# Kernel optimization log

Measured on AMD Instinct MI355X. Metric: run time of the kernel, lower is better.

## Reference

```python
import jax, jax.numpy as jnp
import numpy as np

Q_HEADS = 16
KV_HEADS = 4
ROPE_THETA = 10000.0


def _rope(x, seq_len):
    # x: [B, S, H, D]; pairs are consecutive along D (view_as_complex semantics)
    D = x.shape[-1]
    inv_freq = 1.0 / (ROPE_THETA ** (jnp.arange(0, D, 2, dtype=jnp.float32) / D))
    freqs = jnp.arange(seq_len, dtype=jnp.float32)[:, None] * inv_freq  # [S, D/2]
    cos = jnp.cos(freqs)[None, :, None, :]
    sin = jnp.sin(freqs)[None, :, None, :]
    xr = x.reshape(x.shape[:-1] + (D // 2, 2))
    x0, x1 = xr[..., 0], xr[..., 1]
    out = jnp.stack([x0 * cos - x1 * sin, x0 * sin + x1 * cos], axis=-1)
    return out.reshape(x.shape)


def setup_inputs() -> dict:
    key = jax.random.key(0)
    ks = jax.random.split(key, 6)
    B, S, E = 1, 2048, 2048
    KV_DIM = KV_HEADS * (E // Q_HEADS)  # 512
    scale = 0.02
    return {
        "x": jax.random.normal(ks[0], (B, S, E), dtype=jnp.float32),
        "Wq": jax.random.normal(ks[1], (E, E), dtype=jnp.float32) * scale,
        "Wk": jax.random.normal(ks[2], (KV_DIM, E), dtype=jnp.float32) * scale,
        "Wv": jax.random.normal(ks[3], (KV_DIM, E), dtype=jnp.float32) * scale,
        "Wo": jax.random.normal(ks[4], (E, E), dtype=jnp.float32) * scale,
        "bo": jax.random.normal(ks[5], (E,), dtype=jnp.float32) * scale,
        "cache_keys": jnp.zeros((B, S, KV_HEADS, E // Q_HEADS), dtype=jnp.float32),
        "cache_value": jnp.zeros((B, S, KV_HEADS, E // Q_HEADS), dtype=jnp.float32),
        "start_pos": 0,
    }


def reference(x, Wq, Wk, Wv, Wo, bo, cache_keys, cache_value, start_pos):
    B, S, E = x.shape
    hd = E // Q_HEADS
    G = Q_HEADS // KV_HEADS  # queries per kv head

    xq = (x @ Wq.T).reshape(B, S, Q_HEADS, hd)
    xk = (x @ Wk.T).reshape(B, S, KV_HEADS, hd)
    xv = (x @ Wv.T).reshape(B, S, KV_HEADS, hd)

    # Original applies RoPE with positions 0..seq_len-1 for both q and k
    # (freq tensor is sliced [:seq_len] inside apply_rotry_position_embedding).
    xq = _rope(xq, S)
    xk = _rope(xk, S)

    # cache write at start_pos (static python int)
    cache_keys = jax.lax.dynamic_update_slice(cache_keys, xk, (0, start_pos, 0, 0))
    cache_value = jax.lax.dynamic_update_slice(cache_value, xv, (0, start_pos, 0, 0))
    total = start_pos + S
    k_full = cache_keys[:, :total]   # [B, T, KVH, hd]
    v_full = cache_value[:, :total]

    # repeat_interleave over the head axis == GQA expansion
    k = jnp.repeat(k_full, G, axis=2)  # [B, T, QH, hd]
    v = jnp.repeat(v_full, G, axis=2)

    scores = jnp.einsum("bshd,bthd->bhst", xq, k) / jnp.sqrt(jnp.float32(hd))
    causal = jnp.triu(jnp.ones((S, total), dtype=bool), k=1)  # [S, T]
    scores = jnp.where(causal[None, None, :, :], -jnp.inf, scores)
    weights = jax.nn.softmax(scores, axis=-1)
    out = jnp.einsum("bhst,bthd->bshd", weights, v).reshape(B, S, E)
    # dropout p=0.0 / eval mode -> identity
    return out @ Wo.T + bo
```

## Files before the change

kernel.cpp:

```cpp
#include <hip/hip_runtime.h>
#include <stdint.h>

typedef unsigned short u16;
typedef float  f32x4  __attribute__((ext_vector_type(4)));
typedef __bf16 bf16x8 __attribute__((ext_vector_type(8)));
typedef __bf16 bf16x4 __attribute__((ext_vector_type(4)));
typedef unsigned short u16x8 __attribute__((ext_vector_type(8)));
typedef unsigned short u16x4v __attribute__((ext_vector_type(4)));

#define S_LEN 2048
#define E_DIM 2048
#define HD    128
#define QH    16
#define KVH   4
#define KVD   512
#define NQKV  3072
#define QK_SCALE 0.08838834764831845f

#define AS1 __attribute__((address_space(1)))
#define AS3 __attribute__((address_space(3)))

__device__ __forceinline__ u16 f2bf(float f) {
  union { float f; uint32_t u; } v; v.f = f;
  return (u16)((v.u + 0x7FFFu + ((v.u >> 16) & 1u)) >> 16);
}
__device__ __forceinline__ float bf2f(u16 b) {
  union { uint32_t u; float f; } v; v.u = ((uint32_t)b) << 16;
  return v.f;
}

__global__ void cast_all_kernel(const float* __restrict__ x, const float* __restrict__ Wq,
                                const float* __restrict__ Wk, const float* __restrict__ Wv,
                                const float* __restrict__ Wo,
                                u16* __restrict__ xb, u16* __restrict__ Wcat,
                                u16* __restrict__ Wob) {
  int i = blockIdx.x * blockDim.x + threadIdx.x;
  const float* src; u16* dst;
  if (i < (1 << 20))                       { src = x  + (size_t)i * 4;  dst = xb + (size_t)i * 4; }
  else if (i < (2 << 20))                  { size_t j = i - (1 << 20);  src = Wq + j * 4; dst = Wcat + j * 4; }
  else if (i < (2 << 20) + (1 << 18))      { size_t j = i - (2 << 20);  src = Wk + j * 4; dst = Wcat + (size_t)E_DIM * E_DIM + j * 4; }
  else if (i < (2 << 20) + (2 << 18))      { size_t j = i - (2 << 20) - (1 << 18); src = Wv + j * 4; dst = Wcat + (size_t)(E_DIM + KVD) * E_DIM + j * 4; }
  else                                     { size_t j = i - (2 << 20) - (2 << 18); src = Wo + j * 4; dst = Wob + j * 4; }
  float4 f = *reinterpret_cast<const float4*>(src);
  u16x4v o;
  o[0] = f2bf(f.x); o[1] = f2bf(f.y); o[2] = f2bf(f.z); o[3] = f2bf(f.w);
  *reinterpret_cast<u16x4v*>(dst) = o;
}

template<bool BIAS, bool OBF16>
__global__ __launch_bounds__(256) void gemm_bt_kernel(
    const u16* __restrict__ A, const u16* __restrict__ B,
    void* __restrict__ Cv, const float* __restrict__ bias,
    int M, int N, int K)
{
  __shared__ u16 As[2][128 * 64];
  __shared__ u16 Bs[2][128 * 64];

  const int tid  = threadIdx.x;
  const int lane = tid & 63;
  const int wid  = tid >> 6;
  const int wr   = (wid >> 1) * 64;
  const int wc   = (wid & 1) * 64;
  const int lr   = lane & 15;
  const int kg   = lane >> 4;

  const int bm = blockIdx.y * 128;
  const int bn = blockIdx.x * 128;

  f32x4 acc[4][4];
  #pragma unroll
  for (int r = 0; r < 4; ++r)
    #pragma unroll
    for (int c = 0; c < 4; ++c) acc[r][c] = (f32x4){0.f, 0.f, 0.f, 0.f};

  const int l8 = lane & 7;
  const int l3 = lane >> 3;
  const int schunk = l8 ^ l3;

  const u16* gA = A + (size_t)(bm + wid*32 + l3) * K + schunk * 8;
  const u16* gB = B + (size_t)(bn + wid*32 + l3) * K + schunk * 8;

  const int sw = lr & 7;

  auto stage = [&](int buf, int kt) {
    #pragma unroll
    for (int i = 0; i < 4; ++i) {
      __builtin_amdgcn_global_load_lds(
          (const AS1 void*)(gA + (size_t)i * 8 * K + kt),
          (AS3 void*)(&As[buf][wid*32*64 + i*8*64]), 16, 0, 0);
      __builtin_amdgcn_global_load_lds(
          (const AS1 void*)(gB + (size_t)i * 8 * K + kt),
          (AS3 void*)(&Bs[buf][wid*32*64 + i*8*64]), 16, 0, 0);
    }
  };

  stage(0, 0);
  __syncthreads();

  int cur = 0;
  for (int kt = 0; kt < K; kt += 64) {
    if (kt + 64 < K) stage(cur ^ 1, kt + 64);
    #pragma unroll
    for (int kk = 0; kk < 2; ++kk) {
      bf16x8 af[4], bfr[4];
      #pragma unroll
      for (int r = 0; r < 4; ++r)
        af[r] = *reinterpret_cast<const bf16x8*>(
            &As[cur][(wr + r*16 + lr)*64 + ((kk*4 + kg) ^ sw)*8]);
      #pragma unroll
      for (int c = 0; c < 4; ++c)
        bfr[c] = *reinterpret_cast<const bf16x8*>(
            &Bs[cur][(wc + c*16 + lr)*64 + ((kk*4 + kg) ^ sw)*8]);
      #pragma unroll
      for (int r = 0; r < 4; ++r)
        #pragma unroll
        for (int c = 0; c < 4; ++c)
          acc[r][c] = __builtin_amdgcn_mfma_f32_16x16x32_bf16(af[r], bfr[c], acc[r][c], 0, 0, 0);
    }
    __syncthreads();
    cur ^= 1;
  }

  const int crow = kg * 4;
  #pragma unroll
  for (int r = 0; r < 4; ++r) {
    #pragma unroll
    for (int c = 0; c < 4; ++c) {
      int gr = bm + wr + r*16 + crow;
      int gc = bn + wc + c*16 + lr;
      float badd = BIAS ? bias[gc] : 0.0f;
      #pragma unroll
      for (int reg = 0; reg < 4; ++reg) {
        float v = acc[r][c][reg] + badd;
        if constexpr (OBF16)
          ((u16*)Cv)[(size_t)(gr + reg)*N + gc] = f2bf(v);
        else
          ((float*)Cv)[(size_t)(gr + reg)*N + gc] = v;
      }
    }
  }
}

__global__ void rope_split_kernel(const u16* __restrict__ qkv,
                                  u16* __restrict__ qb, u16* __restrict__ kb) {
  int idx = blockIdx.x * blockDim.x + threadIdx.x;
  int s  = idx / 1280;
  int cp = idx - s * 1280;
  int col = cp * 2;
  const u16* src = qkv + (size_t)s * NQKV + col;
  float x0 = bf2f(src[0]), x1 = bf2f(src[1]);
  int p = (col & 127) >> 1;
  float inv = exp2f((float)p * (-13.287712379549449f / 64.0f));
  float ang = (float)s * inv;
  float sn, cs;
  sincosf(ang, &sn, &cs);
  float o0 = x0 * cs - x1 * sn;
  float o1 = x0 * sn + x1 * cs;
  if (col < E_DIM) {
    o0 *= QK_SCALE; o1 *= QK_SCALE;
    qb[(size_t)s * E_DIM + col]     = f2bf(o0);
    qb[(size_t)s * E_DIM + col + 1] = f2bf(o1);
  } else {
    kb[(size_t)s * KVD + (col - E_DIM)]     = f2bf(o0);
    kb[(size_t)s * KVD + (col - E_DIM) + 1] = f2bf(o1);
  }
}

__global__ void transpose_v_kernel(const u16* __restrict__ qkv, u16* __restrict__ vT) {
  __shared__ u16 tile[32][33];
  const int sbase = blockIdx.x * 32;
  const int cbase = blockIdx.y * 32;
  const int tx = threadIdx.x;
  const int ty = threadIdx.y;
  #pragma unroll
  for (int i = 0; i < 32; i += 8)
    tile[ty + i][tx] = qkv[(size_t)(sbase + ty + i) * NQKV + (E_DIM + KVD) + cbase + tx];
  __syncthreads();
  #pragma unroll
  for (int i = 0; i < 32; i += 8)
    vT[(size_t)(cbase + ty + i) * S_LEN + sbase + tx] = tile[tx][ty + i];
}

__global__ __launch_bounds__(256, 2) void attn_kernel(
    const u16* __restrict__ Q, const u16* __restrict__ Kc,
    const u16* __restrict__ VT, u16* __restrict__ Out)
{
  __shared__ u16 Ks[2][64 * 128];
  __shared__ u16 VTs[128 * 64];
  __shared__ u16 Ps[4][16 * 72];

  const int x    = blockIdx.x;
  const int pp   = x >> 1;
  const int base = pp & 15;
  const int h    = (pp >> 4) & 15;
  const int flip = (x ^ (x >> 8)) & 1;
  const int qt   = flip ? 31 - base : base;
  const int kvh  = h >> 2;

  const int tid  = threadIdx.x;
  const int lane = tid & 63;
  const int wid  = tid >> 6;
  const int lr   = lane & 15;
  const int kg   = lane >> 4;
  const int sw   = lr & 7;

  const int NT = qt + 1;

  bf16x8 qf[4];
  {
    const u16* qa = Q + (size_t)(qt*64 + wid*16 + lr) * E_DIM + h * HD + kg * 8;
    #pragma unroll
    for (int kk = 0; kk < 4; ++kk)
      qf[kk] = *reinterpret_cast<const bf16x8*>(qa + kk * 32);
  }

  f32x4 o[8];
  #pragma unroll
  for (int d = 0; d < 8; ++d) o[d] = (f32x4){0.f,0.f,0.f,0.f};
  float mr = -1e30f, ls = 0.f;

  const u16* kbase = Kc + kvh * HD;
  const u16* vbase = VT + (size_t)(kvh * HD) * S_LEN;
  u16* ps = Ps[wid];

  const int kr_off = lane >> 4;
  const int kchunk = lane & 15;
  auto k_dma = [&](int buf, int t) {
    #pragma unroll
    for (int j = 0; j < 4; ++j) {
      int r0 = j*16 + wid*4;
      int r  = r0 + kr_off;
      const u16* src = kbase + (size_t)(t*64 + r) * KVD + ((kchunk ^ (r & 7)) * 8);
      __builtin_amdgcn_global_load_lds((const AS1 void*)src,
          (AS3 void*)(&Ks[buf][r0 * 128]), 16, 0, 0);
    }
  };

  u16x8 vreg[4];
  auto v_load = [&](int t) {
    #pragma unroll
    for (int i = 0; i < 4; ++i) {
      int c = i * 256 + tid;
      vreg[i] = *reinterpret_cast<const u16x8*>(
          vbase + (size_t)(c >> 3) * S_LEN + t*64 + (c & 7) * 8);
    }
  };
  auto v_write = [&]() {
    #pragma unroll
    for (int i = 0; i < 4; ++i) {
      int c = i * 256 + tid;
      int d = c >> 3;
      *reinterpret_cast<u16x8*>(&VTs[d*64 + ((c & 7) ^ (d & 7)) * 8]) = vreg[i];
    }
  };

  k_dma(0, 0);
  v_load(0);
  v_write();
  __syncthreads();

  int p = 0;
  for (int t = 0; t < NT; ++t) {
    const bool lastt = (t + 1 == NT);
    if (!lastt) { k_dma(p ^ 1, t + 1); v_load(t + 1); }

    f32x4 st[4];
    #pragma unroll
    for (int c = 0; c < 4; ++c) st[c] = (f32x4){0.f, 0.f, 0.f, 0.f};
    __builtin_amdgcn_s_setprio(1);
    #pragma unroll
    for (int kk = 0; kk < 4; ++kk) {
      #pragma unroll
      for (int c = 0; c < 4; ++c) {
        bf16x8 kfr = *reinterpret_cast<const bf16x8*>(
            &Ks[p][(c*16 + lr)*128 + ((kk*4 + kg) ^ sw)*8]);
        st[c] = __builtin_amdgcn_mfma_f32_16x16x32_bf16(kfr, qf[kk], st[c], 0, 0, 0);
      }
    }
    __builtin_amdgcn_s_setprio(0);

    if (t == qt) {
      #pragma unroll
      for (int c = 0; c < 4; ++c)
        #pragma unroll
        for (int reg = 0; reg < 4; ++reg)
          if (c*16 + kg*4 + reg > wid*16 + lr) st[c][reg] = -1e30f;
    }

    float cm[4];
    #pragma unroll
    for (int c = 0; c < 4; ++c)
      cm[c] = fmaxf(fmaxf(st[c][0], st[c][1]), fmaxf(st[c][2], st[c][3]));
    float pm = fmaxf(fmaxf(cm[0], cm[1]), fmaxf(cm[2], cm[3]));
    pm = fmaxf(pm, __shfl_xor(pm, 16));
    pm = fmaxf(pm, __shfl_xor(pm, 32));

    if (!__all(pm - mr <= 8.0f)) {
      float nm = fmaxf(mr, pm);
      float alpha = __expf(mr - nm);
      ls *= alpha;
      mr = nm;
      float ar[4];
      #pragma unroll
      for (int reg = 0; reg < 4; ++reg)
        ar[reg] = __shfl(alpha, kg*4 + reg);
      #pragma unroll
      for (int d = 0; d < 8; ++d)
        #pragma unroll
        for (int reg = 0; reg < 4; ++reg)
          o[d][reg] *= ar[reg];
    }

    float sum = 0.f;
    #pragma unroll
    for (int c = 0; c < 4; ++c) {
      float pr[4];
      #pragma unroll
      for (int reg = 0; reg < 4; ++reg)
        pr[reg] = __expf(st[c][reg] - mr);
      sum += (pr[0] + pr[1]) + (pr[2] + pr[3]);
      bf16x4 pk;
      #pragma unroll
      for (int reg = 0; reg < 4; ++reg) pk[reg] = (__bf16)pr[reg];
      *reinterpret_cast<bf16x4*>(&ps[lr*72 + c*16 + kg*4]) = pk;
    }
    sum += __shfl_xor(sum, 16);
    sum += __shfl_xor(sum, 32);
    ls += sum;

    bf16x8 pa[2];
    #pragma unroll
    for (int kk = 0; kk < 2; ++kk)
      pa[kk] = *reinterpret_cast<const bf16x8*>(&ps[lr*72 + kk*32 + kg*8]);
    __builtin_amdgcn_s_setprio(1);
    #pragma unroll
    for (int d0 = 0; d0 < 8; ++d0) {
      #pragma unroll
      for (int kk = 0; kk < 2; ++kk) {
        bf16x8 vb = *reinterpret_cast<const bf16x8*>(
            &VTs[(d0*16 + lr)*64 + ((kk*4 + kg) ^ sw)*8]);
        o[d0] = __builtin_amdgcn_mfma_f32_16x16x32_bf16(pa[kk], vb, o[d0], 0, 0, 0);
      }
    }
    __builtin_amdgcn_s_setprio(0);

    if (!lastt) {
      __syncthreads();
      v_write();
      __syncthreads();
      p ^= 1;
    }
  }

  {
    float inv = 1.0f / ls;
    float ivq[4];
    #pragma unroll
    for (int reg = 0; reg < 4; ++reg)
      ivq[reg] = __shfl(inv, kg*4 + reg);
    #pragma unroll
    for (int reg = 0; reg < 4; ++reg) {
      int grow = qt*64 + wid*16 + kg*4 + reg;
      #pragma unroll
      for (int d = 0; d < 8; ++d)
        Out[(size_t)grow * E_DIM + h * HD + d*16 + lr] =
            __builtin_bit_cast(u16, (__bf16)(o[d][reg] * ivq[reg]));
    }
  }
}

extern "C" void kernel_launch(void* const* d_in, const int* in_sizes, int n_in,
                              void* d_out, int out_size, void* d_ws, size_t ws_size,
                              hipStream_t stream)
{
  const float* x  = (const float*)d_in[0];
  const float* Wq = (const float*)d_in[1];
  const float* Wk = (const float*)d_in[2];
  const float* Wv = (const float*)d_in[3];
  const float* Wo = (const float*)d_in[4];
  const float* bo = (const float*)d_in[5];
  float* out = (float*)d_out;

  char* w = (char*)d_ws;
  u16*   xb   = (u16*)(w);
  u16*   Wcat = (u16*)(w + (8u  << 20));
  u16*   Wob  = (u16*)(w + (20u << 20));
  u16*   qkv  = (u16*)(w + (28u << 20));
  u16*   qb   = (u16*)(w + (52u << 20));
  u16*   kb   = (u16*)(w + (60u << 20));
  u16*   vT   = (u16*)(w + (62u << 20));
  u16*   attn = (u16*)(w + (64u << 20));
  (void)ws_size; (void)in_sizes; (void)n_in; (void)out_size;

  cast_all_kernel<<<14336, 256, 0, stream>>>(x, Wq, Wk, Wv, Wo, xb, Wcat, Wob);

  gemm_bt_kernel<false, true><<<dim3(NQKV/128, S_LEN/128), 256, 0, stream>>>(
      xb, Wcat, qkv, nullptr, S_LEN, NQKV, E_DIM);

  rope_split_kernel<<<(S_LEN * 1280) / 256, 256, 0, stream>>>(qkv, qb, kb);
  transpose_v_kernel<<<dim3(S_LEN/32, KVD/32), dim3(32, 8), 0, stream>>>(qkv, vT);

  attn_kernel<<<512, 256, 0, stream>>>(qb, kb, vT, attn);

  gemm_bt_kernel<true, false><<<dim3(E_DIM/128, S_LEN/128), 256, 0, stream>>>(
      attn, Wob, out, bo, S_LEN, E_DIM, E_DIM);
}
```

Baseline: 151.5 us.

## Split KV tiles across two wave groups per attention block and merge

```diff
diff --git a/kernel.cpp b/kernel.cpp
--- a/kernel.cpp
+++ b/kernel.cpp
@@ -181,34 +181,37 @@
     vT[(size_t)(cbase + ty + i) * S_LEN + sbase + tx] = tile[tx][ty + i];
 }
 
-__global__ __launch_bounds__(256, 2) void attn_kernel(
+__global__ __launch_bounds__(512, 1) void attn_kernel(
     const u16* __restrict__ Q, const u16* __restrict__ Kc,
     const u16* __restrict__ VT, u16* __restrict__ Out)
 {
-  __shared__ u16 Ks[2][64 * 128];
-  __shared__ u16 VTs[128 * 64];
-  __shared__ u16 Ps[4][16 * 72];
-
-  const int x    = blockIdx.x;
-  const int pp   = x >> 1;
-  const int base = pp & 15;
-  const int h    = (pp >> 4) & 15;
-  const int flip = (x ^ (x >> 8)) & 1;
-  const int qt   = flip ? 31 - base : base;
-  const int kvh  = h >> 2;
+  __shared__ u16 Ks[2][2][64 * 128];
+  __shared__ u16 VTs[2][128 * 64];
+  __shared__ u16 Ps[8][16 * 72];
+  __shared__ float Lm[4][16], Ll[4][16];
+
+  const int x = blockIdx.x;
+  int qt, h;
+  if (x < 256) { qt = 31 - (x & 15); h = x >> 4; }
+  else         { int y = x - 256; qt = 15 - (y & 15); h = y >> 4; }
+  const int kvh = h >> 2;
 
   const int tid  = threadIdx.x;
   const int lane = tid & 63;
   const int wid  = tid >> 6;
+  const int grp  = wid >> 2;
+  const int wl   = wid & 3;
+  const int ltid = tid & 255;
   const int lr   = lane & 15;
   const int kg   = lane >> 4;
   const int sw   = lr & 7;
 
   const int NT = qt + 1;
+  const int NI = (NT + 1) >> 1;
 
   bf16x8 qf[4];
   {
-    const u16* qa = Q + (size_t)(qt*64 + wid*16 + lr) * E_DIM + h * HD + kg * 8;
+    const u16* qa = Q + (size_t)(qt*64 + wl*16 + lr) * E_DIM + h * HD + kg * 8;
     #pragma unroll
     for (int kk = 0; kk < 4; ++kk)
       qf[kk] = *reinterpret_cast<const bf16x8*>(qa + kk * 32);
@@ -228,11 +231,11 @@
   auto k_dma = [&](int buf, int t) {
     #pragma unroll
     for (int j = 0; j < 4; ++j) {
-      int r0 = j*16 + wid*4;
+      int r0 = j*16 + wl*4;
       int r  = r0 + kr_off;
       const u16* src = kbase + (size_t)(t*64 + r) * KVD + ((kchunk ^ (r & 7)) * 8);
       __builtin_amdgcn_global_load_lds((const AS1 void*)src,
-          (AS3 void*)(&Ks[buf][r0 * 128]), 16, 0, 0);
+          (AS3 void*)(&Ks[grp][buf][r0 * 128]), 16, 0, 0);
     }
   };
 
@@ -240,7 +243,7 @@
   auto v_load = [&](int t) {
     #pragma unroll
     for (int i = 0; i < 4; ++i) {
-      int c = i * 256 + tid;
+      int c = i * 256 + ltid;
       vreg[i] = *reinterpret_cast<const u16x8*>(
           vbase + (size_t)(c >> 3) * S_LEN + t*64 + (c & 7) * 8);
     }
@@ -248,123 +251,151 @@
   auto v_write = [&]() {
     #pragma unroll
     for (int i = 0; i < 4; ++i) {
-      int c = i * 256 + tid;
+      int c = i * 256 + ltid;
       int d = c >> 3;
-      *reinterpret_cast<u16x8*>(&VTs[d*64 + ((c & 7) ^ (d & 7)) * 8]) = vreg[i];
+      *reinterpret_cast<u16x8*>(&VTs[grp][d*64 + ((c & 7) ^ (d & 7)) * 8]) = vreg[i];
     }
   };
 
-  k_dma(0, 0);
-  v_load(0);
-  v_write();
+  if (grp < NT) {
+    k_dma(0, grp);
+    v_load(grp);
+    v_write();
+  }
   __syncthreads();
 
   int p = 0;
-  for (int t = 0; t < NT; ++t) {
-    const bool lastt = (t + 1 == NT);
-    if (!lastt) { k_dma(p ^ 1, t + 1); v_load(t + 1); }
-
-    f32x4 st[4];
-    #pragma unroll
-    for (int c = 0; c < 4; ++c) st[c] = (f32x4){0.f, 0.f, 0.f, 0.f};
-    __builtin_amdgcn_s_setprio(1);
-    #pragma unroll
-    for (int kk = 0; kk < 4; ++kk) {
+  for (int i = 0; i < NI; ++i) {
+    const int t = 2*i + grp;
+    const bool valid = t < NT;
+    const bool hn = t + 2 < NT;
+    if (valid && hn) { k_dma(p ^ 1, t + 2); v_load(t + 2); }
+
+    if (valid) {
+      f32x4 st[4];
+      #pragma unroll
+      for (int c = 0; c < 4; ++c) st[c] = (f32x4){0.f, 0.f, 0.f, 0.f};
+      __builtin_amdgcn_s_setprio(1);
+      #pragma unroll
+      for (int kk = 0; kk < 4; ++kk) {
+        #pragma unroll
+        for (int c = 0; c < 4; ++c) {
+          bf16x8 kfr = *reinterpret_cast<const bf16x8*>(
+              &Ks[grp][p][(c*16 + lr)*128 + ((kk*4 + kg) ^ sw)*8]);
+          st[c] = __builtin_amdgcn_mfma_f32_16x16x32_bf16(kfr, qf[kk], st[c], 0, 0, 0);
+        }
+      }
+      __builtin_amdgcn_s_setprio(0);
+
+      if (t == qt) {
+        #pragma unroll
+        for (int c = 0; c < 4; ++c)
+          #pragma unroll
+          for (int reg = 0; reg < 4; ++reg)
+            if (c*16 + kg*4 + reg > wl*16 + lr) st[c][reg] = -1e30f;
+      }
+
+      float cm[4];
+      #pragma unroll
+      for (int c = 0; c < 4; ++c)
+        cm[c] = fmaxf(fmaxf(st[c][0], st[c][1]), fmaxf(st[c][2], st[c][3]));
+      float pm = fmaxf(fmaxf(cm[0], cm[1]), fmaxf(cm[2], cm[3]));
+      pm = fmaxf(pm, __shfl_xor(pm, 16));
+      pm = fmaxf(pm, __shfl_xor(pm, 32));
+
+      if (!__all(pm - mr <= 8.0f)) {
+        float nm = fmaxf(mr, pm);
+        float alpha = __expf(mr - nm);
+        ls *= alpha;
+        mr = nm;
+        float ar[4];
+        #pragma unroll
+        for (int reg = 0; reg < 4; ++reg)
+          ar[reg] = __shfl(alpha, kg*4 + reg);
+        #pragma unroll
+        for (int d = 0; d < 8; ++d)
+          #pragma unroll
+          for (int reg = 0; reg < 4; ++reg)
+            o[d][reg] *= ar[reg];
+      }
+
+      float sum = 0.f;
       #pragma unroll
       for (int c = 0; c < 4; ++c) {
-        bf16x8 kfr = *reinterpret_cast<const bf16x8*>(
-            &Ks[p][(c*16 + lr)*128 + ((kk*4 + kg) ^ sw)*8]);
-        st[c] = __builtin_amdgcn_mfma_f32_16x16x32_bf16(kfr, qf[kk], st[c], 0, 0, 0);
-      }
-    }
-    __builtin_amdgcn_s_setprio(0);
-
-    if (t == qt) {
-      #pragma unroll
-      for (int c = 0; c < 4; ++c)
+        float pr[4];
         #pragma unroll
         for (int reg = 0; reg < 4; ++reg)
-          if (c*16 + kg*4 + reg > wid*16 + lr) st[c][reg] = -1e30f;
-    }
-
-    float cm[4];
-    #pragma unroll
-    for (int c = 0; c < 4; ++c)
-      cm[c] = fmaxf(fmaxf(st[c][0], st[c][1]), fmaxf(st[c][2], st[c][3]));
-    float pm = fmaxf(fmaxf(cm[0], cm[1]), fmaxf(cm[2], cm[3]));
-    pm = fmaxf(pm, __shfl_xor(pm, 16));
-    pm = fmaxf(pm, __shfl_xor(pm, 32));
-
-    if (!__all(pm - mr <= 8.0f)) {
-      float nm = fmaxf(mr, pm);
-      float alpha = __expf(mr - nm);
-      ls *= alpha;
-      mr = nm;
-      float ar[4];
-      #pragma unroll
-      for (int reg = 0; reg < 4; ++reg)
-        ar[reg] = __shfl(alpha, kg*4 + reg);
-      #pragma unroll
-      for (int d = 0; d < 8; ++d)
-        #pragma unroll
-        for (int reg = 0; reg < 4; ++reg)
-          o[d][reg] *= ar[reg];
-    }
-
-    float sum = 0.f;
-    #pragma unroll
-    for (int c = 0; c < 4; ++c) {
-      float pr[4];
-      #pragma unroll
-      for (int reg = 0; reg < 4; ++reg)
-        pr[reg] = __expf(st[c][reg] - mr);
-      sum += (pr[0] + pr[1]) + (pr[2] + pr[3]);
-      bf16x4 pk;
-      #pragma unroll
-      for (int reg = 0; reg < 4; ++reg) pk[reg] = (__bf16)pr[reg];
-      *reinterpret_cast<bf16x4*>(&ps[lr*72 + c*16 + kg*4]) = pk;
-    }
-    sum += __shfl_xor(sum, 16);
-    sum += __shfl_xor(sum, 32);
-    ls += sum;
-
-    bf16x8 pa[2];
-    #pragma unroll
-    for (int kk = 0; kk < 2; ++kk)
-      pa[kk] = *reinterpret_cast<const bf16x8*>(&ps[lr*72 + kk*32 + kg*8]);
-    __builtin_amdgcn_s_setprio(1);
-    #pragma unroll
-    for (int d0 = 0; d0 < 8; ++d0) {
-      #pragma unroll
-      for (int kk = 0; kk < 2; ++kk) {
-        bf16x8 vb = *reinterpret_cast<const bf16x8*>(
-            &VTs[(d0*16 + lr)*64 + ((kk*4 + kg) ^ sw)*8]);
-        o[d0] = __builtin_amdgcn_mfma_f32_16x16x32_bf16(pa[kk], vb, o[d0], 0, 0, 0);
-      }
-    }
-    __builtin_amdgcn_s_setprio(0);
-
-    if (!lastt) {
+          pr[reg] = __expf(st[c][reg] - mr);
+        sum += (pr[0] + pr[1]) + (pr[2] + pr[3]);
+        bf16x4 pk;
+        #pragma unroll
+        for (int reg = 0; reg < 4; ++reg) pk[reg] = (__bf16)pr[reg];
+        *reinterpret_cast<bf16x4*>(&ps[lr*72 + c*16 + kg*4]) = pk;
+      }
+      sum += __shfl_xor(sum, 16);
+      sum += __shfl_xor(sum, 32);
+      ls += sum;
+
+      bf16x8 pa[2];
+      #pragma unroll
+      for (int kk = 0; kk < 2; ++kk)
+        pa[kk] = *reinterpret_cast<const bf16x8*>(&ps[lr*72 + kk*32 + kg*8]);
+      __builtin_amdgcn_s_setprio(1);
+      #pragma unroll
+      for (int d0 = 0; d0 < 8; ++d0) {
+        #pragma unroll
+        for (int kk = 0; kk < 2; ++kk) {
+          bf16x8 vb = *reinterpret_cast<const bf16x8*>(
+              &VTs[grp][(d0*16 + lr)*64 + ((kk*4 + kg) ^ sw)*8]);
+          o[d0] = __builtin_amdgcn_mfma_f32_16x16x32_bf16(pa[kk], vb, o[d0], 0, 0, 0);
+        }
+      }
+      __builtin_amdgcn_s_setprio(0);
+    }
+
+    if (i + 1 < NI) {
       __syncthreads();
-      v_write();
+      if (hn) v_write();
       __syncthreads();
       p ^= 1;
     }
   }
 
-  {
-    float inv = 1.0f / ls;
-    float ivq[4];
-    #pragma unroll
-    for (int reg = 0; reg < 4; ++reg)
-      ivq[reg] = __shfl(inv, kg*4 + reg);
+  __syncthreads();
+  float* Obuf = (float*)&Ks[0][0][0];
+  if (grp == 1) {
+    if (kg == 0) { Lm[wl][lr] = mr; Ll[wl][lr] = ls; }
     #pragma unroll
     for (int reg = 0; reg < 4; ++reg) {
-      int grow = qt*64 + wid*16 + kg*4 + reg;
+      int rrow = wl*16 + kg*4 + reg;
       #pragma unroll
       for (int d = 0; d < 8; ++d)
+        Obuf[rrow*128 + d*16 + lr] = o[d][reg];
+    }
+  }
+  __syncthreads();
+  if (grp == 0) {
+    float m0r[4], l0r[4];
+    #pragma unroll
+    for (int reg = 0; reg < 4; ++reg) {
+      m0r[reg] = __shfl(mr, kg*4 + reg);
+      l0r[reg] = __shfl(ls, kg*4 + reg);
+    }
+    #pragma unroll
+    for (int reg = 0; reg < 4; ++reg) {
+      int rloc = kg*4 + reg;
+      float m1 = Lm[wl][rloc], l1 = Ll[wl][rloc];
+      float m  = fmaxf(m0r[reg], m1);
+      float a0 = __expf(m0r[reg] - m);
+      float a1 = __expf(m1 - m);
+      float inv = 1.0f / (l0r[reg]*a0 + l1*a1);
+      int grow = qt*64 + wl*16 + rloc;
+      #pragma unroll
+      for (int d = 0; d < 8; ++d) {
+        float v = (o[d][reg]*a0 + Obuf[(wl*16 + rloc)*128 + d*16 + lr]*a1) * inv;
         Out[(size_t)grow * E_DIM + h * HD + d*16 + lr] =
-            __builtin_bit_cast(u16, (__bf16)(o[d][reg] * ivq[reg]));
+            __builtin_bit_cast(u16, (__bf16)v);
+      }
     }
   }
 }
@@ -400,7 +431,7 @@
   rope_split_kernel<<<(S_LEN * 1280) / 256, 256, 0, stream>>>(qkv, qb, kb);
   transpose_v_kernel<<<dim3(S_LEN/32, KVD/32), dim3(32, 8), 0, stream>>>(qkv, vT);
 
-  attn_kernel<<<512, 256, 0, stream>>>(qb, kb, vT, attn);
+  attn_kernel<<<512, 512, 0, stream>>>(qb, kb, vT, attn);
 
   gemm_bt_kernel<true, false><<<dim3(E_DIM/128, S_LEN/128), 256, 0, stream>>>(
       attn, Wob, out, bo, S_LEN, E_DIM, E_DIM);
```

After: 161.5 us. +6.6%, slower.

## Switch attention to 32x32x16 MFMA with two waves per block

Applied to the files above, without the earlier changes.

```diff
diff --git a/kernel.cpp b/kernel.cpp
--- a/kernel.cpp
+++ b/kernel.cpp
@@ -3,6 +3,7 @@
 
 typedef unsigned short u16;
 typedef float  f32x4  __attribute__((ext_vector_type(4)));
+typedef float  f32x16 __attribute__((ext_vector_type(16)));
 typedef __bf16 bf16x8 __attribute__((ext_vector_type(8)));
 typedef __bf16 bf16x4 __attribute__((ext_vector_type(4)));
 typedef unsigned short u16x8 __attribute__((ext_vector_type(8)));
@@ -181,13 +182,13 @@
     vT[(size_t)(cbase + ty + i) * S_LEN + sbase + tx] = tile[tx][ty + i];
 }
 
-__global__ __launch_bounds__(256, 2) void attn_kernel(
+__global__ __launch_bounds__(128) void attn_kernel(
     const u16* __restrict__ Q, const u16* __restrict__ Kc,
     const u16* __restrict__ VT, u16* __restrict__ Out)
 {
   __shared__ u16 Ks[2][64 * 128];
   __shared__ u16 VTs[128 * 64];
-  __shared__ u16 Ps[4][16 * 72];
+  __shared__ u16 Ps[2][32 * 72];
 
   const int x    = blockIdx.x;
   const int pp   = x >> 1;
@@ -200,23 +201,24 @@
   const int tid  = threadIdx.x;
   const int lane = tid & 63;
   const int wid  = tid >> 6;
-  const int lr   = lane & 15;
-  const int kg   = lane >> 4;
-  const int sw   = lr & 7;
+  const int ln   = lane & 31;
+  const int hi   = lane >> 5;
 
   const int NT = qt + 1;
 
-  bf16x8 qf[4];
+  bf16x8 qf[8];
   {
-    const u16* qa = Q + (size_t)(qt*64 + wid*16 + lr) * E_DIM + h * HD + kg * 8;
-    #pragma unroll
-    for (int kk = 0; kk < 4; ++kk)
-      qf[kk] = *reinterpret_cast<const bf16x8*>(qa + kk * 32);
-  }
-
-  f32x4 o[8];
+    const u16* qa = Q + (size_t)(qt*64 + wid*32 + ln) * E_DIM + h * HD + hi * 8;
+    #pragma unroll
+    for (int ks = 0; ks < 8; ++ks)
+      qf[ks] = *reinterpret_cast<const bf16x8*>(qa + ks * 16);
+  }
+
+  f32x16 o4[4];
   #pragma unroll
-  for (int d = 0; d < 8; ++d) o[d] = (f32x4){0.f,0.f,0.f,0.f};
+  for (int d = 0; d < 4; ++d)
+    #pragma unroll
+    for (int r = 0; r < 16; ++r) o4[d][r] = 0.f;
   float mr = -1e30f, ls = 0.f;
 
   const u16* kbase = Kc + kvh * HD;
@@ -227,8 +229,8 @@
   const int kchunk = lane & 15;
   auto k_dma = [&](int buf, int t) {
     #pragma unroll
-    for (int j = 0; j < 4; ++j) {
-      int r0 = j*16 + wid*4;
+    for (int j = 0; j < 8; ++j) {
+      int r0 = j*8 + wid*4;
       int r  = r0 + kr_off;
       const u16* src = kbase + (size_t)(t*64 + r) * KVD + ((kchunk ^ (r & 7)) * 8);
       __builtin_amdgcn_global_load_lds((const AS1 void*)src,
@@ -236,19 +238,19 @@
     }
   };
 
-  u16x8 vreg[4];
+  u16x8 vreg[8];
   auto v_load = [&](int t) {
     #pragma unroll
-    for (int i = 0; i < 4; ++i) {
-      int c = i * 256 + tid;
+    for (int i = 0; i < 8; ++i) {
+      int c = i * 128 + tid;
       vreg[i] = *reinterpret_cast<const u16x8*>(
           vbase + (size_t)(c >> 3) * S_LEN + t*64 + (c & 7) * 8);
     }
   };
   auto v_write = [&]() {
     #pragma unroll
-    for (int i = 0; i < 4; ++i) {
-      int c = i * 256 + tid;
+    for (int i = 0; i < 8; ++i) {
+      int c = i * 128 + tid;
       int d = c >> 3;
       *reinterpret_cast<u16x8*>(&VTs[d*64 + ((c & 7) ^ (d & 7)) * 8]) = vreg[i];
     }
@@ -264,35 +266,39 @@
     const bool lastt = (t + 1 == NT);
     if (!lastt) { k_dma(p ^ 1, t + 1); v_load(t + 1); }
 
-    f32x4 st[4];
-    #pragma unroll
-    for (int c = 0; c < 4; ++c) st[c] = (f32x4){0.f, 0.f, 0.f, 0.f};
+    f32x16 st[2];
+    #pragma unroll
+    for (int c = 0; c < 2; ++c)
+      #pragma unroll
+      for (int r = 0; r < 16; ++r) st[c][r] = 0.f;
     __builtin_amdgcn_s_setprio(1);
     #pragma unroll
-    for (int kk = 0; kk < 4; ++kk) {
-      #pragma unroll
-      for (int c = 0; c < 4; ++c) {
+    for (int ks = 0; ks < 8; ++ks) {
+      #pragma unroll
+      for (int c = 0; c < 2; ++c) {
+        int row = c*32 + ln;
         bf16x8 kfr = *reinterpret_cast<const bf16x8*>(
-            &Ks[p][(c*16 + lr)*128 + ((kk*4 + kg) ^ sw)*8]);
-        st[c] = __builtin_amdgcn_mfma_f32_16x16x32_bf16(kfr, qf[kk], st[c], 0, 0, 0);
+            &Ks[p][row*128 + ((ks*2 + hi) ^ (row & 7))*8]);
+        st[c] = __builtin_amdgcn_mfma_f32_32x32x16_bf16(kfr, qf[ks], st[c], 0, 0, 0);
       }
     }
     __builtin_amdgcn_s_setprio(0);
 
     if (t == qt) {
       #pragma unroll
-      for (int c = 0; c < 4; ++c)
+      for (int c = 0; c < 2; ++c)
         #pragma unroll
-        for (int reg = 0; reg < 4; ++reg)
-          if (c*16 + kg*4 + reg > wid*16 + lr) st[c][reg] = -1e30f;
-    }
-
-    float cm[4];
-    #pragma unroll
-    for (int c = 0; c < 4; ++c)
-      cm[c] = fmaxf(fmaxf(st[c][0], st[c][1]), fmaxf(st[c][2], st[c][3]));
-    float pm = fmaxf(fmaxf(cm[0], cm[1]), fmaxf(cm[2], cm[3]));
-    pm = fmaxf(pm, __shfl_xor(pm, 16));
+        for (int reg = 0; reg < 16; ++reg) {
+          int kvl = c*32 + (reg & 3) + 8*(reg >> 2) + 4*hi;
+          if (kvl > wid*32 + ln) st[c][reg] = -1e30f;
+        }
+    }
+
+    float pm = -1e30f;
+    #pragma unroll
+    for (int c = 0; c < 2; ++c)
+      #pragma unroll
+      for (int reg = 0; reg < 16; ++reg) pm = fmaxf(pm, st[c][reg]);
     pm = fmaxf(pm, __shfl_xor(pm, 32));
 
     if (!__all(pm - mr <= 8.0f)) {
@@ -300,46 +306,47 @@
       float alpha = __expf(mr - nm);
       ls *= alpha;
       mr = nm;
-      float ar[4];
-      #pragma unroll
-      for (int reg = 0; reg < 4; ++reg)
-        ar[reg] = __shfl(alpha, kg*4 + reg);
-      #pragma unroll
-      for (int d = 0; d < 8; ++d)
+      #pragma unroll
+      for (int reg = 0; reg < 16; ++reg) {
+        int crow = (reg & 3) + 8*(reg >> 2) + 4*hi;
+        float ar = __shfl(alpha, crow);
         #pragma unroll
-        for (int reg = 0; reg < 4; ++reg)
-          o[d][reg] *= ar[reg];
+        for (int d = 0; d < 4; ++d) o4[d][reg] *= ar;
+      }
     }
 
     float sum = 0.f;
     #pragma unroll
-    for (int c = 0; c < 4; ++c) {
-      float pr[4];
-      #pragma unroll
-      for (int reg = 0; reg < 4; ++reg)
-        pr[reg] = __expf(st[c][reg] - mr);
-      sum += (pr[0] + pr[1]) + (pr[2] + pr[3]);
-      bf16x4 pk;
-      #pragma unroll
-      for (int reg = 0; reg < 4; ++reg) pk[reg] = (__bf16)pr[reg];
-      *reinterpret_cast<bf16x4*>(&ps[lr*72 + c*16 + kg*4]) = pk;
-    }
-    sum += __shfl_xor(sum, 16);
+    for (int c = 0; c < 2; ++c) {
+      #pragma unroll
+      for (int rg = 0; rg < 4; ++rg) {
+        float pr[4];
+        #pragma unroll
+        for (int j = 0; j < 4; ++j)
+          pr[j] = __expf(st[c][rg*4 + j] - mr);
+        sum += (pr[0] + pr[1]) + (pr[2] + pr[3]);
+        bf16x4 pk;
+        #pragma unroll
+        for (int j = 0; j < 4; ++j) pk[j] = (__bf16)pr[j];
+        *reinterpret_cast<bf16x4*>(&ps[ln*72 + c*32 + rg*8 + hi*4]) = pk;
+      }
+    }
     sum += __shfl_xor(sum, 32);
     ls += sum;
 
-    bf16x8 pa[2];
-    #pragma unroll
-    for (int kk = 0; kk < 2; ++kk)
-      pa[kk] = *reinterpret_cast<const bf16x8*>(&ps[lr*72 + kk*32 + kg*8]);
+    bf16x8 pa[4];
+    #pragma unroll
+    for (int ks = 0; ks < 4; ++ks)
+      pa[ks] = *reinterpret_cast<const bf16x8*>(&ps[ln*72 + ks*16 + hi*8]);
     __builtin_amdgcn_s_setprio(1);
     #pragma unroll
-    for (int d0 = 0; d0 < 8; ++d0) {
-      #pragma unroll
-      for (int kk = 0; kk < 2; ++kk) {
+    for (int d = 0; d < 4; ++d) {
+      #pragma unroll
+      for (int ks = 0; ks < 4; ++ks) {
+        int row = d*32 + ln;
         bf16x8 vb = *reinterpret_cast<const bf16x8*>(
-            &VTs[(d0*16 + lr)*64 + ((kk*4 + kg) ^ sw)*8]);
-        o[d0] = __builtin_amdgcn_mfma_f32_16x16x32_bf16(pa[kk], vb, o[d0], 0, 0, 0);
+            &VTs[row*64 + ((ks*2 + hi) ^ (row & 7))*8]);
+        o4[d] = __builtin_amdgcn_mfma_f32_32x32x16_bf16(pa[ks], vb, o4[d], 0, 0, 0);
       }
     }
     __builtin_amdgcn_s_setprio(0);
@@ -354,17 +361,15 @@
 
   {
     float inv = 1.0f / ls;
-    float ivq[4];
-    #pragma unroll
-    for (int reg = 0; reg < 4; ++reg)
-      ivq[reg] = __shfl(inv, kg*4 + reg);
-    #pragma unroll
-    for (int reg = 0; reg < 4; ++reg) {
-      int grow = qt*64 + wid*16 + kg*4 + reg;
-      #pragma unroll
-      for (int d = 0; d < 8; ++d)
-        Out[(size_t)grow * E_DIM + h * HD + d*16 + lr] =
-            __builtin_bit_cast(u16, (__bf16)(o[d][reg] * ivq[reg]));
+    #pragma unroll
+    for (int reg = 0; reg < 16; ++reg) {
+      int crow = (reg & 3) + 8*(reg >> 2) + 4*hi;
+      float iv = __shfl(inv, crow);
+      int grow = qt*64 + wid*32 + crow;
+      #pragma unroll
+      for (int d = 0; d < 4; ++d)
+        Out[(size_t)grow * E_DIM + h * HD + d*32 + ln] =
+            __builtin_bit_cast(u16, (__bf16)(o4[d][reg] * iv));
     }
   }
 }
@@ -400,7 +405,7 @@
   rope_split_kernel<<<(S_LEN * 1280) / 256, 256, 0, stream>>>(qkv, qb, kb);
   transpose_v_kernel<<<dim3(S_LEN/32, KVD/32), dim3(32, 8), 0, stream>>>(qkv, vT);
 
-  attn_kernel<<<512, 256, 0, stream>>>(qb, kb, vT, attn);
+  attn_kernel<<<512, 128, 0, stream>>>(qb, kb, vT, attn);
 
   gemm_bt_kernel<true, false><<<dim3(E_DIM/128, S_LEN/128), 256, 0, stream>>>(
       attn, Wob, out, bo, S_LEN, E_DIM, E_DIM);
```

Result: slower. 173.7 us (+14.6%).
